# Kernel tuning notes

Measured on AMD Instinct MI355X. Metric: run time of the kernel, lower is better.

The kernel has to match this reference:

```python
import jax, jax.numpy as jnp
import numpy as np

B, C, N = 8, 128, 4096
C2 = C // 2
BN_EPS = 1e-5


def setup_inputs() -> dict:
    key = jax.random.key(0)
    ks = jax.random.split(key, 8)
    s = 1.0 / np.sqrt(C)
    s2 = 1.0 / np.sqrt(C2)
    return {
        "x": jax.random.normal(ks[0], (B, C, N), dtype=jnp.float32),
        "w_qk": jax.random.uniform(ks[1], (C2, C), jnp.float32, -s, s),  # shared q/k weight
        "w_v": jax.random.uniform(ks[2], (C2, C), jnp.float32, -s, s),
        "b_v": jax.random.uniform(ks[3], (C2,), jnp.float32, -s, s),
        "w_x": jax.random.uniform(ks[4], (C2, C), jnp.float32, -s, s),
        "w_t": jax.random.uniform(ks[5], (C2, C2), jnp.float32, -s2, s2),
        "b_t": jax.random.uniform(ks[6], (C2,), jnp.float32, -s2, s2),
        "gamma": jnp.ones((C2,), jnp.float32),
        "beta": jnp.zeros((C2,), jnp.float32),
    }


def reference(x, w_qk, w_v, b_v, w_x, w_t, b_t, gamma, beta):
    # 1x1 convs are per-point linear maps: [B,C,N] -> [B,C2,N]
    x_q = jnp.einsum("oc,bcn->bno", w_qk, x)          # [B, N, C2]
    x_k = jnp.einsum("oc,bcn->bon", w_qk, x)          # [B, C2, N]
    x_v = jnp.einsum("oc,bcn->bon", w_v, x) + b_v[None, :, None]

    energy = jnp.einsum("bno,bom->bnm", x_q, x_k)     # [B, N, N]
    attn = jax.nn.softmax(energy, axis=-1)            # row softmax
    attn = attn / (1e-9 + attn.sum(axis=1, keepdims=True))  # column L1 renorm

    x_r = jnp.einsum("bon,bnm->bom", x_v, attn)       # [B, C2, N]
    x_c = jnp.einsum("oc,bcn->bon", w_x, x)           # [B, C2, N]

    d = x_c - x_r
    t = jnp.einsum("oi,bin->bon", w_t, d) + b_t[None, :, None]
    # BatchNorm1d (training-mode batch stats) over (B, N) per channel
    mean = t.mean(axis=(0, 2), keepdims=True)
    var = t.var(axis=(0, 2), keepdims=True)
    t_hat = (t - mean) * jax.lax.rsqrt(var + BN_EPS)
    x_r2 = jax.nn.relu(gamma[None, :, None] * t_hat + beta[None, :, None])
    return x_c + x_r2
```

## Files before the change

### kernel.cpp

```cpp
#include <hip/hip_runtime.h>

#define B_   8
#define C_   128
#define N_   4096
#define C2_  64

typedef __bf16 bf16x8 __attribute__((ext_vector_type(8)));
typedef float  f32x4  __attribute__((ext_vector_type(4)));

#define MFMA16(a, b, c) __builtin_amdgcn_mfma_f32_16x16x32_bf16((a), (b), (c), 0, 0, 0)

#define QK_SCALE 1.2011224087864498f

static __device__ __forceinline__ unsigned short f2bf(float f) {
    union { __bf16 b; unsigned short u; } cv;
    cv.b = (__bf16)f;
    return cv.u;
}
static __device__ __forceinline__ float bf2f(unsigned short u) {
    union { unsigned int u; float f; } cv;
    cv.u = ((unsigned int)u) << 16;
    return cv.f;
}

struct us4 { unsigned short a, b, c, d; };

static __device__ __forceinline__ void gl_lds16(const unsigned short* g, void* l) {
    __builtin_amdgcn_global_load_lds(
        (const __attribute__((address_space(1))) unsigned int*)g,
        (__attribute__((address_space(3))) unsigned int*)l,
        16, 0, 0);
}

__global__ __launch_bounds__(256) void k1_proj(
    const float* __restrict__ x, const float* __restrict__ w_qk,
    const float* __restrict__ w_v, const float* __restrict__ b_v,
    const float* __restrict__ w_x,
    unsigned short* __restrict__ qk_t, unsigned short* __restrict__ xv_bf,
    float* __restrict__ xc)
{
    __shared__ __align__(16) unsigned short w_lds[192 * 136];
    __shared__ __align__(16) unsigned short x_t[64 * 136];
    const int tid = threadIdx.x;
    const int wave = tid >> 6, lane = tid & 63;
    const int quad = lane >> 4, col = lane & 15;
    const int b = blockIdx.y;
    const int n0 = blockIdx.x * 64;

    const float* wsrc[3] = {w_qk, w_v, w_x};
    #pragma unroll
    for (int mat = 0; mat < 3; ++mat) {
        const float* wm = wsrc[mat];
        #pragma unroll
        for (int it = 0; it < 8; ++it) {
            const int idx = it * 256 + tid;
            const int o = idx >> 5, c = (idx & 31) * 4;
            const float4 v = *(const float4*)(wm + o * C_ + c);
            us4 pk;
            pk.a = f2bf(v.x); pk.b = f2bf(v.y); pk.c = f2bf(v.z); pk.d = f2bf(v.w);
            *(us4*)&w_lds[(mat * 64 + o) * 136 + c] = pk;
        }
    }
    const float* xb = x + (size_t)b * C_ * N_ + n0;
    #pragma unroll
    for (int it = 0; it < 8; ++it) {
        const int idx = it * 256 + tid;
        const int c = idx >> 4, n = (idx & 15) * 4;
        const float4 v = *(const float4*)(xb + (size_t)c * N_ + n);
        x_t[(n + 0) * 136 + c] = f2bf(v.x);
        x_t[(n + 1) * 136 + c] = f2bf(v.y);
        x_t[(n + 2) * 136 + c] = f2bf(v.z);
        x_t[(n + 3) * 136 + c] = f2bf(v.w);
    }
    __syncthreads();

    const int nw = wave * 16;
    bf16x8 bfr[4];
    #pragma unroll
    for (int kt = 0; kt < 4; ++kt)
        bfr[kt] = *(const bf16x8*)&x_t[(nw + col) * 136 + kt * 32 + quad * 8];

    const int n_g = n0 + nw + col;

    #pragma unroll
    for (int ot = 0; ot < 12; ++ot) {
        f32x4 acc = {0.f, 0.f, 0.f, 0.f};
        #pragma unroll
        for (int kt = 0; kt < 4; ++kt) {
            const bf16x8 afr = *(const bf16x8*)&w_lds[(ot * 16 + col) * 136 + kt * 32 + quad * 8];
            acc = MFMA16(afr, bfr[kt], acc);
        }
        if (ot < 4) {
            us4 pk;
            pk.a = f2bf(acc[0] * QK_SCALE); pk.b = f2bf(acc[1] * QK_SCALE);
            pk.c = f2bf(acc[2] * QK_SCALE); pk.d = f2bf(acc[3] * QK_SCALE);
            *(us4*)&qk_t[(size_t)(b * N_ + n_g) * C2_ + ot * 16 + quad * 4] = pk;
        } else if (ot < 8) {
            const float4 bv4 = *(const float4*)(b_v + (ot - 4) * 16 + quad * 4);
            const float* bvp = (const float*)&bv4;
            #pragma unroll
            for (int r = 0; r < 4; ++r)
                xv_bf[(size_t)(b * C2_ + (ot - 4) * 16 + quad * 4 + r) * N_ + n_g]
                    = f2bf(acc[r] + bvp[r]);
        } else {
            #pragma unroll
            for (int r = 0; r < 4; ++r)
                xc[(size_t)(b * C2_ + (ot - 8) * 16 + quad * 4 + r) * N_ + n_g] = acc[r];
        }
    }
}

__global__ __launch_bounds__(256) void k2_rowstats(
    const unsigned short* __restrict__ qk_t, float* __restrict__ part_rs)
{
    __shared__ __align__(16) unsigned char lds_raw[2 * 8192];
    const int tid = threadIdx.x;
    const int wave = tid >> 6, lane = tid & 63;
    const int quad = lane >> 4, col = lane & 15;
    const int b = blockIdx.x & 7;
    const int nblk = (blockIdx.x >> 3) & 15;
    const int mq = blockIdx.x >> 7;
    const int n_base = nblk * 256 + wave * 64;
    const int m_start = mq * 512;
    const unsigned short* qb = qk_t + (size_t)b * N_ * C2_;

    bf16x8 a0[4], a1[4];
    #pragma unroll
    for (int s = 0; s < 4; ++s) {
        const unsigned short* p = qb + (size_t)(n_base + s * 16 + col) * C2_ + quad * 8;
        a0[s] = *(const bf16x8*)p;
        a1[s] = *(const bf16x8*)(p + 32);
    }

    auto stage = [&](int m0, int p) {
        unsigned char* base = lds_raw + p * 8192;
        #pragma unroll
        for (int r = 0; r < 2; ++r) {
            const int idx = r * 256 + tid;
            const int row = idx >> 3, seg = idx & 7;
            gl_lds16(qb + (size_t)(m0 + row) * C2_ + (size_t)(seg ^ (row & 7)) * 8,
                     base + idx * 16);
        }
    };

    float run_s[4][4];
    #pragma unroll
    for (int s = 0; s < 4; ++s)
        #pragma unroll
        for (int r = 0; r < 4; ++r) run_s[s][r] = 0.f;

    stage(m_start, 0);
    __syncthreads();

    for (int c = 0; c < 8; ++c) {
        const int p = c & 1;
        if (c + 1 < 8) stage(m_start + (c + 1) * 64, 1 - p);
        const unsigned short* qt = (const unsigned short*)(lds_raw + p * 8192);
        #pragma unroll
        for (int ms = 0; ms < 4; ++ms) {
            const int row = ms * 16 + col;
            const bf16x8 b0 = *(const bf16x8*)(qt + row * 64 + ((quad ^ (col & 7)) * 8));
            const bf16x8 b1 = *(const bf16x8*)(qt + row * 64 + (((4 + quad) ^ (col & 7)) * 8));
            #pragma unroll
            for (int s = 0; s < 4; ++s) {
                f32x4 acc = {0.f, 0.f, 0.f, 0.f};
                acc = MFMA16(a0[s], b0, acc);
                acc = MFMA16(a1[s], b1, acc);
                #pragma unroll
                for (int r = 0; r < 4; ++r)
                    run_s[s][r] += __builtin_amdgcn_exp2f(acc[r]);
            }
        }
        __syncthreads();
    }

    #pragma unroll
    for (int s = 0; s < 4; ++s)
        #pragma unroll
        for (int r = 0; r < 4; ++r) {
            #pragma unroll
            for (int off = 1; off < 16; off <<= 1)
                run_s[s][r] += __shfl_xor(run_s[s][r], off, 64);
        }
    if (col == 0) {
        #pragma unroll
        for (int s = 0; s < 4; ++s)
            #pragma unroll
            for (int r = 0; r < 4; ++r)
                part_rs[((size_t)(mq * 8 + b) << 12) + n_base + s * 16 + quad * 4 + r]
                    = run_s[s][r];
    }
}

__global__ __launch_bounds__(256) void k2b_comb(
    const float* __restrict__ part_rs, float* __restrict__ winv,
    unsigned short* __restrict__ wbf)
{
    const int i = blockIdx.x * 256 + threadIdx.x;
    const int b = i >> 12, n = i & 4095;
    float s = 0.f;
    #pragma unroll
    for (int q = 0; q < 8; ++q)
        s += part_rs[((size_t)(q * 8 + b) << 12) + n];
    const float w = 1.0f / s;
    winv[i] = w;
    wbf[i] = f2bf(w);
}

__global__ __launch_bounds__(256) void k2c_scale(
    unsigned short* __restrict__ xv_bf, const float* __restrict__ winv)
{
    const int t = blockIdx.x * 256 + threadIdx.x;
    const int flat = t * 4;
    const int b = flat >> 18;
    const int n = flat & 4095;
    const float4 w4 = *(const float4*)(winv + b * 4096 + n);
    us4 v = *(us4*)(xv_bf + flat);
    v.a = f2bf(bf2f(v.a) * w4.x);
    v.b = f2bf(bf2f(v.b) * w4.y);
    v.c = f2bf(bf2f(v.c) * w4.z);
    v.d = f2bf(bf2f(v.d) * w4.w);
    *(us4*)(xv_bf + flat) = v;
}

__global__ __launch_bounds__(256, 3) void k3_pv(
    const unsigned short* __restrict__ qk_t, const unsigned short* __restrict__ xv_bf,
    const unsigned short* __restrict__ wbf,
    float* __restrict__ yp0, float* __restrict__ yp1, float* __restrict__ yp2,
    float* __restrict__ cspart)
{
    __shared__ __align__(16) unsigned char lds_raw[32768 + 4 * 5120];
    const int tid = threadIdx.x;
    const int wave = tid >> 6, lane = tid & 63;
    const int quad = lane >> 4, col = lane & 15;
    const int nh2 = wave & 1, mh = wave >> 1;
    const int b = blockIdx.x & 7;
    const int m_blk = ((blockIdx.x >> 3) & 31) * 128;
    const int sk = blockIdx.x >> 8;
    const int n_start = (sk == 0) ? 0 : 1408 + (sk - 1) * 1344;
    const int n_chunks = (sk == 0) ? 22 : 21;
    const int m_wave = m_blk + mh * 64;
    const unsigned short* qb = qk_t + (size_t)b * N_ * C2_;
    const unsigned short* vb = xv_bf + (size_t)b * C2_ * N_;
    const unsigned short* wb = wbf + b * N_;
    float* yp = (sk == 0) ? yp0 : (sk == 1) ? yp1 : yp2;

    bf16x8 kb0[4], kb1[4];
    #pragma unroll
    for (int g = 0; g < 4; ++g) {
        const unsigned short* p = qb + (size_t)(m_wave + g * 16 + col) * C2_ + quad * 8;
        kb0[g] = *(const bf16x8*)p;
        kb1[g] = *(const bf16x8*)(p + 32);
    }

    unsigned short* stS = (unsigned short*)(lds_raw + 32768 + wave * 5120);

    auto stage = [&](int n0, int p) {
        unsigned char* qbase = lds_raw + p * 8192;
        unsigned char* vbase = lds_raw + 16384 + p * 8192;
        #pragma unroll
        for (int r = 0; r < 2; ++r) {
            const int idx = r * 256 + tid;
            const int row = idx >> 3, seg = idx & 7;
            const int ss = seg ^ (row & 7);
            gl_lds16(qb + (size_t)(n0 + row) * C2_ + (size_t)ss * 8, qbase + idx * 16);
            gl_lds16(vb + (size_t)row * N_ + n0 + ss * 8, vbase + idx * 16);
        }
    };

    f32x4 accY[4][4];
    #pragma unroll
    for (int g = 0; g < 4; ++g)
        #pragma unroll
        for (int os = 0; os < 4; ++os) accY[g][os] = (f32x4){0.f, 0.f, 0.f, 0.f};
    f32x4 csacc[4];
    #pragma unroll
    for (int g = 0; g < 4; ++g) csacc[g] = (f32x4){0.f, 0.f, 0.f, 0.f};

    stage(n_start, 0);
    __syncthreads();

    for (int c = 0; c < n_chunks; ++c) {
        const int n0 = n_start + c * 64;
        const int p = c & 1;
        if (c + 1 < n_chunks) stage(n0 + 64, 1 - p);

        const unsigned short* qt = (const unsigned short*)(lds_raw + p * 8192);
        const unsigned short* vt = (const unsigned short*)(lds_raw + 16384 + p * 8192);

        const bf16x8 wfrag = *(const bf16x8*)(wb + n0 + nh2 * 32 + quad * 8);

        #pragma unroll
        for (int ns = 0; ns < 2; ++ns) {
            const int row = nh2 * 32 + ns * 16 + col;
            const bf16x8 qa0 = *(const bf16x8*)(qt + row * 64 + ((quad ^ (col & 7)) * 8));
            const bf16x8 qa1 = *(const bf16x8*)(qt + row * 64 + (((4 + quad) ^ (col & 7)) * 8));
            #pragma unroll
            for (int g = 0; g < 4; ++g) {
                f32x4 acc = {0.f, 0.f, 0.f, 0.f};
                acc = MFMA16(qa0, kb0[g], acc);
                acc = MFMA16(qa1, kb1[g], acc);
                union { unsigned short us[4]; uint2 u2; } pk;
                #pragma unroll
                for (int r = 0; r < 4; ++r)
                    pk.us[r] = f2bf(__builtin_amdgcn_exp2f(acc[r]));
                *(uint2*)&stS[(g * 16 + col) * 40 + ns * 16 + quad * 4] = pk.u2;
            }
        }

        bf16x8 sB[4];
        #pragma unroll
        for (int g = 0; g < 4; ++g)
            sB[g] = *(const bf16x8*)&stS[(g * 16 + col) * 40 + quad * 8];

        #pragma unroll
        for (int g = 0; g < 4; ++g)
            csacc[g] = MFMA16(wfrag, sB[g], csacc[g]);

        #pragma unroll
        for (int os = 0; os < 4; ++os) {
            const bf16x8 va = *(const bf16x8*)(vt + (os * 16 + col) * 64 +
                                               (((nh2 * 4 + quad) ^ (col & 7)) * 8));
            #pragma unroll
            for (int g = 0; g < 4; ++g)
                accY[g][os] = MFMA16(va, sB[g], accY[g][os]);
        }
        __syncthreads();
    }

    float* cmb = (float*)lds_raw;
    float* csc = (float*)(lds_raw + 32768);
    if (nh2 == 1) {
        #pragma unroll
        for (int g = 0; g < 4; ++g) {
            #pragma unroll
            for (int os = 0; os < 4; ++os)
                #pragma unroll
                for (int r = 0; r < 4; ++r)
                    cmb[((mh * 16 + g * 4 + os) * 4 + r) * 64 + lane] = accY[g][os][r];
            csc[(mh * 4 + g) * 64 + lane] = csacc[g][0];
        }
    }
    __syncthreads();
    if (nh2 == 0) {
        #pragma unroll
        for (int g = 0; g < 4; ++g) {
            const float cs = csacc[g][0] + csc[(mh * 4 + g) * 64 + lane];
            if (lane < 16)
                cspart[((size_t)sk * 8 + b) * N_ + m_wave + g * 16 + lane] = cs;
            #pragma unroll
            for (int os = 0; os < 4; ++os)
                #pragma unroll
                for (int r = 0; r < 4; ++r) {
                    const float v = accY[g][os][r] +
                        cmb[((mh * 16 + g * 4 + os) * 4 + r) * 64 + lane];
                    yp[(size_t)(b * C2_ + os * 16 + quad * 4 + r) * N_ + m_wave + g * 16 + col] = v;
                }
        }
    }
}

__global__ __launch_bounds__(256) void k3b_comb(
    float* yp0, const float* __restrict__ yp1, const float* __restrict__ yp2,
    const float* __restrict__ cspart)
{
    const int idx4 = blockIdx.x * 256 + threadIdx.x;
    const int b = idx4 >> 16;
    const int m4 = idx4 & 1023;
    const float4 y0 = ((const float4*)yp0)[idx4];
    const float4 y1 = ((const float4*)yp1)[idx4];
    const float4 y2 = ((const float4*)yp2)[idx4];
    const float4 c0 = ((const float4*)cspart)[b * 1024 + m4];
    const float4 c1 = ((const float4*)cspart)[8192 + b * 1024 + m4];
    const float4 c2 = ((const float4*)cspart)[16384 + b * 1024 + m4];
    float4 r;
    r.x = (y0.x + y1.x + y2.x) / (1e-9f + c0.x + c1.x + c2.x);
    r.y = (y0.y + y1.y + y2.y) / (1e-9f + c0.y + c1.y + c2.y);
    r.z = (y0.z + y1.z + y2.z) / (1e-9f + c0.z + c1.z + c2.z);
    r.w = (y0.w + y1.w + y2.w) / (1e-9f + c0.w + c1.w + c2.w);
    ((float4*)yp0)[idx4] = r;
}

__global__ __launch_bounds__(256) void k4_t(
    const float* __restrict__ xc, const float* __restrict__ xr,
    const float* __restrict__ w_t, const float* __restrict__ b_t,
    float* __restrict__ t_buf)
{
    __shared__ float d_lds[64][64];
    __shared__ float w_lds[64][64];
    const int b = blockIdx.y;
    const int n0 = blockIdx.x * 64;
    const size_t base = (size_t)b * C2_ * N_;

    for (int idx = threadIdx.x; idx < 4096; idx += 256) {
        const int i = idx >> 6, n = idx & 63;
        const size_t g = base + (size_t)i * N_ + n0 + n;
        d_lds[i][n] = xc[g] - xr[g];
        w_lds[i][n] = w_t[idx];
    }
    __syncthreads();

    const int n = threadIdx.x & 63, ow = (threadIdx.x >> 6) * 16;
    float acc[16];
    #pragma unroll
    for (int oo = 0; oo < 16; ++oo) acc[oo] = 0.f;
    for (int i = 0; i < 64; ++i) {
        const float dv = d_lds[i][n];
        #pragma unroll
        for (int oo = 0; oo < 16; ++oo)
            acc[oo] += w_lds[ow + oo][i] * dv;
    }
    #pragma unroll
    for (int oo = 0; oo < 16; ++oo)
        t_buf[base + (size_t)(ow + oo) * N_ + n0 + n] = acc[oo] + b_t[ow + oo];
}

__global__ __launch_bounds__(256) void k5_bnstats(
    const float* __restrict__ t_buf, float* __restrict__ bn)
{
    const int o = blockIdx.x;
    float s = 0.f, s2 = 0.f;
    for (int b = 0; b < B_; ++b) {
        const float4* p = (const float4*)(t_buf + (size_t)(b * C2_ + o) * N_);
        for (int j = threadIdx.x; j < N_ / 4; j += 256) {
            const float4 v = p[j];
            s  += v.x + v.y + v.z + v.w;
            s2 += v.x * v.x + v.y * v.y + v.z * v.z + v.w * v.w;
        }
    }
    #pragma unroll
    for (int off = 1; off < 64; off <<= 1) {
        s  += __shfl_xor(s, off, 64);
        s2 += __shfl_xor(s2, off, 64);
    }
    __shared__ float red[2][4];
    if ((threadIdx.x & 63) == 0) {
        red[0][threadIdx.x >> 6] = s;
        red[1][threadIdx.x >> 6] = s2;
    }
    __syncthreads();
    if (threadIdx.x == 0) {
        bn[o]       = red[0][0] + red[0][1] + red[0][2] + red[0][3];
        bn[64 + o]  = red[1][0] + red[1][1] + red[1][2] + red[1][3];
    }
}

__global__ __launch_bounds__(256) void k6_out(
    const float* __restrict__ xc, const float* __restrict__ t_buf,
    const float* __restrict__ bn, const float* __restrict__ gamma,
    const float* __restrict__ beta, float* __restrict__ out)
{
    const int idx = blockIdx.x * 256 + threadIdx.x;
    const int o = (idx >> 10) & 63;
    const float invC = 1.0f / (float)(B_ * N_);
    const float mean = bn[o] * invC;
    const float var  = bn[64 + o] * invC - mean * mean;
    const float sc = gamma[o] * rsqrtf(var + 1e-5f);
    const float sh = beta[o] - mean * sc;
    const float4 t4 = ((const float4*)t_buf)[idx];
    const float4 c4 = ((const float4*)xc)[idx];
    float4 r;
    r.x = c4.x + fmaxf(0.f, sc * t4.x + sh);
    r.y = c4.y + fmaxf(0.f, sc * t4.y + sh);
    r.z = c4.z + fmaxf(0.f, sc * t4.z + sh);
    r.w = c4.w + fmaxf(0.f, sc * t4.w + sh);
    ((float4*)out)[idx] = r;
}

extern "C" void kernel_launch(void* const* d_in, const int* in_sizes, int n_in,
                              void* d_out, int out_size, void* d_ws, size_t ws_size,
                              hipStream_t stream) {
    const float* x     = (const float*)d_in[0];
    const float* w_qk  = (const float*)d_in[1];
    const float* w_v   = (const float*)d_in[2];
    const float* b_v   = (const float*)d_in[3];
    const float* w_x   = (const float*)d_in[4];
    const float* w_t   = (const float*)d_in[5];
    const float* b_t   = (const float*)d_in[6];
    const float* gamma = (const float*)d_in[7];
    const float* beta  = (const float*)d_in[8];
    float* out = (float*)d_out;

    char* ws = (char*)d_ws;
    unsigned short* qk_t  = (unsigned short*)ws;
    unsigned short* xv_bf = (unsigned short*)(ws + (4  << 20));
    float* xc      = (float*)(ws + (8  << 20));
    float* xr_yp0  = (float*)(ws + (16 << 20));
    float* tb_yp1  = (float*)(ws + (24 << 20));
    float* part_rs = (float*)(ws + (32 << 20));
    float* cspart  = (float*)(ws + (32 << 20));
    float* winv    = (float*)(ws + (33 << 20));
    unsigned short* wbf = (unsigned short*)(ws + (33 << 20) + (128 << 10));
    float* bn      = (float*)(ws + (33 << 20) + (192 << 10));
    float* yp2     = out;

    hipLaunchKernelGGL(k1_proj,     dim3(64, 8),  256, 0, stream,
                       x, w_qk, w_v, b_v, w_x, qk_t, xv_bf, xc);
    hipLaunchKernelGGL(k2_rowstats, dim3(1024),   256, 0, stream, qk_t, part_rs);
    hipLaunchKernelGGL(k2b_comb,    dim3(128),    256, 0, stream, part_rs, winv, wbf);
    hipLaunchKernelGGL(k2c_scale,   dim3(2048),   256, 0, stream, xv_bf, winv);
    hipLaunchKernelGGL(k3_pv,       dim3(768),    256, 0, stream,
                       qk_t, xv_bf, wbf, xr_yp0, tb_yp1, yp2, cspart);
    hipLaunchKernelGGL(k3b_comb,    dim3(2048),   256, 0, stream, xr_yp0, tb_yp1, yp2, cspart);
    hipLaunchKernelGGL(k4_t,        dim3(64, 8),  256, 0, stream, xc, xr_yp0, w_t, b_t, tb_yp1);
    hipLaunchKernelGGL(k5_bnstats,  dim3(64),     256, 0, stream, tb_yp1, bn);
    hipLaunchKernelGGL(k6_out,      dim3(2048),   256, 0, stream, xc, tb_yp1, bn, gamma, beta, out);
}
```

Measured before the change: 192.7 us.

## Fuse combine, scaling and BN-stat kernels; use MFMA for the transform conv

Merges the row-sum combine and the V-scaling kernels into one kernel that keeps per-column weights in LDS. Folds the split-K combine and column renormalisation into the transform kernel, which now runs its 64x64 matmul on bf16 MFMA and emits partial BatchNorm sums, so the full-tensor stats pass becomes a small reduction over partials. The row-stats kernel now stages 128-row chunks instead of 64. The intent is fewer launches and fewer full passes over the intermediates, at the cost of bf16 rounding of the difference tensor and in-place aliasing of y1 with t_buf.

```diff
diff --git a/kernel.cpp b/kernel.cpp
--- a/kernel.cpp
+++ b/kernel.cpp
@@ -113,7 +113,7 @@
 __global__ __launch_bounds__(256) void k2_rowstats(
     const unsigned short* __restrict__ qk_t, float* __restrict__ part_rs)
 {
-    __shared__ __align__(16) unsigned char lds_raw[2 * 8192];
+    __shared__ __align__(16) unsigned char lds_raw[2 * 16384];
     const int tid = threadIdx.x;
     const int wave = tid >> 6, lane = tid & 63;
     const int quad = lane >> 4, col = lane & 15;
@@ -133,9 +133,9 @@
     }
 
     auto stage = [&](int m0, int p) {
-        unsigned char* base = lds_raw + p * 8192;
-        #pragma unroll
-        for (int r = 0; r < 2; ++r) {
+        unsigned char* base = lds_raw + p * 16384;
+        #pragma unroll
+        for (int r = 0; r < 4; ++r) {
             const int idx = r * 256 + tid;
             const int row = idx >> 3, seg = idx & 7;
             gl_lds16(qb + (size_t)(m0 + row) * C2_ + (size_t)(seg ^ (row & 7)) * 8,
@@ -152,12 +152,12 @@
     stage(m_start, 0);
     __syncthreads();
 
-    for (int c = 0; c < 8; ++c) {
+    for (int c = 0; c < 4; ++c) {
         const int p = c & 1;
-        if (c + 1 < 8) stage(m_start + (c + 1) * 64, 1 - p);
-        const unsigned short* qt = (const unsigned short*)(lds_raw + p * 8192);
-        #pragma unroll
-        for (int ms = 0; ms < 4; ++ms) {
+        if (c + 1 < 4) stage(m_start + (c + 1) * 128, 1 - p);
+        const unsigned short* qt = (const unsigned short*)(lds_raw + p * 16384);
+        #pragma unroll
+        for (int ms = 0; ms < 8; ++ms) {
             const int row = ms * 16 + col;
             const bf16x8 b0 = *(const bf16x8*)(qt + row * 64 + ((quad ^ (col & 7)) * 8));
             const bf16x8 b1 = *(const bf16x8*)(qt + row * 64 + (((4 + quad) ^ (col & 7)) * 8));
@@ -192,35 +192,36 @@
     }
 }
 
-__global__ __launch_bounds__(256) void k2b_comb(
-    const float* __restrict__ part_rs, float* __restrict__ winv,
+__global__ __launch_bounds__(256) void k2bc(
+    const float* __restrict__ part_rs, unsigned short* __restrict__ xv_bf,
     unsigned short* __restrict__ wbf)
 {
-    const int i = blockIdx.x * 256 + threadIdx.x;
-    const int b = i >> 12, n = i & 4095;
-    float s = 0.f;
-    #pragma unroll
-    for (int q = 0; q < 8; ++q)
-        s += part_rs[((size_t)(q * 8 + b) << 12) + n];
-    const float w = 1.0f / s;
-    winv[i] = w;
-    wbf[i] = f2bf(w);
-}
-
-__global__ __launch_bounds__(256) void k2c_scale(
-    unsigned short* __restrict__ xv_bf, const float* __restrict__ winv)
-{
-    const int t = blockIdx.x * 256 + threadIdx.x;
-    const int flat = t * 4;
-    const int b = flat >> 18;
-    const int n = flat & 4095;
-    const float4 w4 = *(const float4*)(winv + b * 4096 + n);
-    us4 v = *(us4*)(xv_bf + flat);
-    v.a = f2bf(bf2f(v.a) * w4.x);
-    v.b = f2bf(bf2f(v.b) * w4.y);
-    v.c = f2bf(bf2f(v.c) * w4.z);
-    v.d = f2bf(bf2f(v.d) * w4.w);
-    *(us4*)(xv_bf + flat) = v;
+    __shared__ float wl[64];
+    const int tid = threadIdx.x;
+    const int b = blockIdx.x & 7;
+    const int n0 = (blockIdx.x >> 3) * 64;
+    if (tid < 64) {
+        float s = 0.f;
+        #pragma unroll
+        for (int q = 0; q < 8; ++q)
+            s += part_rs[((size_t)(q * 8 + b) << 12) + n0 + tid];
+        const float w = 1.0f / s;
+        wl[tid] = w;
+        wbf[b * N_ + n0 + tid] = f2bf(w);
+    }
+    __syncthreads();
+    #pragma unroll
+    for (int it = 0; it < 4; ++it) {
+        const int idx4 = it * 256 + tid;
+        const int o = idx4 >> 4, n4 = (idx4 & 15) * 4;
+        unsigned short* p = xv_bf + (size_t)(b * C2_ + o) * N_ + n0 + n4;
+        us4 v = *(us4*)p;
+        v.a = f2bf(bf2f(v.a) * wl[n4 + 0]);
+        v.b = f2bf(bf2f(v.b) * wl[n4 + 1]);
+        v.c = f2bf(bf2f(v.c) * wl[n4 + 2]);
+        v.d = f2bf(bf2f(v.d) * wl[n4 + 3]);
+        *(us4*)p = v;
+    }
 }
 
 __global__ __launch_bounds__(256, 3) void k3_pv(
@@ -360,89 +361,112 @@
     }
 }
 
-__global__ __launch_bounds__(256) void k3b_comb(
-    float* yp0, const float* __restrict__ yp1, const float* __restrict__ yp2,
-    const float* __restrict__ cspart)
-{
-    const int idx4 = blockIdx.x * 256 + threadIdx.x;
-    const int b = idx4 >> 16;
-    const int m4 = idx4 & 1023;
-    const float4 y0 = ((const float4*)yp0)[idx4];
-    const float4 y1 = ((const float4*)yp1)[idx4];
-    const float4 y2 = ((const float4*)yp2)[idx4];
-    const float4 c0 = ((const float4*)cspart)[b * 1024 + m4];
-    const float4 c1 = ((const float4*)cspart)[8192 + b * 1024 + m4];
-    const float4 c2 = ((const float4*)cspart)[16384 + b * 1024 + m4];
-    float4 r;
-    r.x = (y0.x + y1.x + y2.x) / (1e-9f + c0.x + c1.x + c2.x);
-    r.y = (y0.y + y1.y + y2.y) / (1e-9f + c0.y + c1.y + c2.y);
-    r.z = (y0.z + y1.z + y2.z) / (1e-9f + c0.z + c1.z + c2.z);
-    r.w = (y0.w + y1.w + y2.w) / (1e-9f + c0.w + c1.w + c2.w);
-    ((float4*)yp0)[idx4] = r;
-}
-
 __global__ __launch_bounds__(256) void k4_t(
-    const float* __restrict__ xc, const float* __restrict__ xr,
-    const float* __restrict__ w_t, const float* __restrict__ b_t,
-    float* __restrict__ t_buf)
-{
-    __shared__ float d_lds[64][64];
-    __shared__ float w_lds[64][64];
+    const float* __restrict__ xc, const float* __restrict__ y0,
+    const float* __restrict__ y1, const float* __restrict__ y2,
+    const float* __restrict__ cspart, const float* __restrict__ w_t,
+    const float* __restrict__ b_t, float* __restrict__ t_buf,
+    float* __restrict__ part_bn)
+{
+    __shared__ __align__(16) unsigned short wlds[64 * 72];
+    __shared__ __align__(16) unsigned short d_t[64 * 72];
+    __shared__ float cinv[64];
+    const int tid = threadIdx.x;
+    const int wave = tid >> 6, lane = tid & 63;
+    const int quad = lane >> 4, col = lane & 15;
     const int b = blockIdx.y;
     const int n0 = blockIdx.x * 64;
     const size_t base = (size_t)b * C2_ * N_;
 
-    for (int idx = threadIdx.x; idx < 4096; idx += 256) {
-        const int i = idx >> 6, n = idx & 63;
-        const size_t g = base + (size_t)i * N_ + n0 + n;
-        d_lds[i][n] = xc[g] - xr[g];
-        w_lds[i][n] = w_t[idx];
-    }
-    __syncthreads();
-
-    const int n = threadIdx.x & 63, ow = (threadIdx.x >> 6) * 16;
-    float acc[16];
-    #pragma unroll
-    for (int oo = 0; oo < 16; ++oo) acc[oo] = 0.f;
-    for (int i = 0; i < 64; ++i) {
-        const float dv = d_lds[i][n];
-        #pragma unroll
-        for (int oo = 0; oo < 16; ++oo)
-            acc[oo] += w_lds[ow + oo][i] * dv;
-    }
-    #pragma unroll
-    for (int oo = 0; oo < 16; ++oo)
-        t_buf[base + (size_t)(ow + oo) * N_ + n0 + n] = acc[oo] + b_t[ow + oo];
-}
-
-__global__ __launch_bounds__(256) void k5_bnstats(
-    const float* __restrict__ t_buf, float* __restrict__ bn)
-{
-    const int o = blockIdx.x;
-    float s = 0.f, s2 = 0.f;
-    for (int b = 0; b < B_; ++b) {
-        const float4* p = (const float4*)(t_buf + (size_t)(b * C2_ + o) * N_);
-        for (int j = threadIdx.x; j < N_ / 4; j += 256) {
-            const float4 v = p[j];
-            s  += v.x + v.y + v.z + v.w;
-            s2 += v.x * v.x + v.y * v.y + v.z * v.z + v.w * v.w;
-        }
-    }
-    #pragma unroll
-    for (int off = 1; off < 64; off <<= 1) {
-        s  += __shfl_xor(s, off, 64);
-        s2 += __shfl_xor(s2, off, 64);
-    }
-    __shared__ float red[2][4];
-    if ((threadIdx.x & 63) == 0) {
-        red[0][threadIdx.x >> 6] = s;
-        red[1][threadIdx.x >> 6] = s2;
-    }
-    __syncthreads();
-    if (threadIdx.x == 0) {
-        bn[o]       = red[0][0] + red[0][1] + red[0][2] + red[0][3];
-        bn[64 + o]  = red[1][0] + red[1][1] + red[1][2] + red[1][3];
-    }
+    #pragma unroll
+    for (int it = 0; it < 4; ++it) {
+        const int idx4 = it * 256 + tid;
+        const int o = idx4 >> 4, i4 = (idx4 & 15) * 4;
+        const float4 v = *(const float4*)(w_t + o * 64 + i4);
+        us4 pk;
+        pk.a = f2bf(v.x); pk.b = f2bf(v.y); pk.c = f2bf(v.z); pk.d = f2bf(v.w);
+        *(us4*)&wlds[o * 72 + i4] = pk;
+    }
+    if (tid < 64) {
+        const int n = n0 + tid;
+        const float cs = cspart[(size_t)b * N_ + n] + cspart[(size_t)(8 + b) * N_ + n]
+                       + cspart[(size_t)(16 + b) * N_ + n];
+        cinv[tid] = 1.0f / (1e-9f + cs);
+    }
+    __syncthreads();
+
+    #pragma unroll
+    for (int it = 0; it < 4; ++it) {
+        const int idx4 = it * 256 + tid;
+        const int i = idx4 >> 4, n4 = (idx4 & 15) * 4;
+        const size_t g = base + (size_t)i * N_ + n0 + n4;
+        const float4 c4 = *(const float4*)(xc + g);
+        const float4 a0 = *(const float4*)(y0 + g);
+        const float4 a1 = *(const float4*)(y1 + g);
+        const float4 a2 = *(const float4*)(y2 + g);
+        d_t[(n4 + 0) * 72 + i] = f2bf(c4.x - (a0.x + a1.x + a2.x) * cinv[n4 + 0]);
+        d_t[(n4 + 1) * 72 + i] = f2bf(c4.y - (a0.y + a1.y + a2.y) * cinv[n4 + 1]);
+        d_t[(n4 + 2) * 72 + i] = f2bf(c4.z - (a0.z + a1.z + a2.z) * cinv[n4 + 2]);
+        d_t[(n4 + 3) * 72 + i] = f2bf(c4.w - (a0.w + a1.w + a2.w) * cinv[n4 + 3]);
+    }
+    __syncthreads();
+
+    const int ow = wave * 16;
+    bf16x8 afr[2];
+    #pragma unroll
+    for (int kt = 0; kt < 2; ++kt)
+        afr[kt] = *(const bf16x8*)&wlds[(ow + col) * 72 + kt * 32 + quad * 8];
+    const float4 bt4 = *(const float4*)(b_t + ow + quad * 4);
+    const float* btp = (const float*)&bt4;
+
+    float s[4] = {0.f, 0.f, 0.f, 0.f}, q2[4] = {0.f, 0.f, 0.f, 0.f};
+    #pragma unroll
+    for (int ns = 0; ns < 4; ++ns) {
+        f32x4 acc = {0.f, 0.f, 0.f, 0.f};
+        #pragma unroll
+        for (int kt = 0; kt < 2; ++kt) {
+            const bf16x8 bfr = *(const bf16x8*)&d_t[(ns * 16 + col) * 72 + kt * 32 + quad * 8];
+            acc = MFMA16(afr[kt], bfr, acc);
+        }
+        #pragma unroll
+        for (int r = 0; r < 4; ++r) {
+            const float t = acc[r] + btp[r];
+            t_buf[base + (size_t)(ow + quad * 4 + r) * N_ + n0 + ns * 16 + col] = t;
+            s[r] += t;
+            q2[r] += t * t;
+        }
+    }
+    #pragma unroll
+    for (int r = 0; r < 4; ++r) {
+        #pragma unroll
+        for (int off = 1; off < 16; off <<= 1) {
+            s[r]  += __shfl_xor(s[r],  off, 64);
+            q2[r] += __shfl_xor(q2[r], off, 64);
+        }
+    }
+    if (col == 0) {
+        const int blk = blockIdx.x * 8 + b;
+        #pragma unroll
+        for (int r = 0; r < 4; ++r) {
+            part_bn[(size_t)(ow + quad * 4 + r) * 512 + blk]      = s[r];
+            part_bn[(size_t)(64 + ow + quad * 4 + r) * 512 + blk] = q2[r];
+        }
+    }
+}
+
+__global__ __launch_bounds__(256) void k5r(
+    const float* __restrict__ part_bn, float* __restrict__ bn)
+{
+    const int c = blockIdx.x;
+    const int tid = threadIdx.x, wave = tid >> 6, lane = tid & 63;
+    float s = 0.f;
+    for (int j = tid; j < 512; j += 256) s += part_bn[(size_t)c * 512 + j];
+    #pragma unroll
+    for (int off = 1; off < 64; off <<= 1) s += __shfl_xor(s, off, 64);
+    __shared__ float red[4];
+    if (lane == 0) red[wave] = s;
+    __syncthreads();
+    if (tid == 0) bn[c] = red[0] + red[1] + red[2] + red[3];
 }
 
 __global__ __launch_bounds__(256) void k6_out(
@@ -485,24 +509,23 @@
     unsigned short* qk_t  = (unsigned short*)ws;
     unsigned short* xv_bf = (unsigned short*)(ws + (4  << 20));
     float* xc      = (float*)(ws + (8  << 20));
-    float* xr_yp0  = (float*)(ws + (16 << 20));
+    float* yp0     = (float*)(ws + (16 << 20));
     float* tb_yp1  = (float*)(ws + (24 << 20));
     float* part_rs = (float*)(ws + (32 << 20));
     float* cspart  = (float*)(ws + (32 << 20));
-    float* winv    = (float*)(ws + (33 << 20));
-    unsigned short* wbf = (unsigned short*)(ws + (33 << 20) + (128 << 10));
-    float* bn      = (float*)(ws + (33 << 20) + (192 << 10));
+    unsigned short* wbf = (unsigned short*)(ws + (33 << 20));
+    float* part_bn = (float*)(ws + (33 << 20) + (64 << 10));
+    float* bn      = (float*)(ws + (33 << 20) + (320 << 10));
     float* yp2     = out;
 
     hipLaunchKernelGGL(k1_proj,     dim3(64, 8),  256, 0, stream,
                        x, w_qk, w_v, b_v, w_x, qk_t, xv_bf, xc);
     hipLaunchKernelGGL(k2_rowstats, dim3(1024),   256, 0, stream, qk_t, part_rs);
-    hipLaunchKernelGGL(k2b_comb,    dim3(128),    256, 0, stream, part_rs, winv, wbf);
-    hipLaunchKernelGGL(k2c_scale,   dim3(2048),   256, 0, stream, xv_bf, winv);
+    hipLaunchKernelGGL(k2bc,        dim3(512),    256, 0, stream, part_rs, xv_bf, wbf);
     hipLaunchKernelGGL(k3_pv,       dim3(768),    256, 0, stream,
-                       qk_t, xv_bf, wbf, xr_yp0, tb_yp1, yp2, cspart);
-    hipLaunchKernelGGL(k3b_comb,    dim3(2048),   256, 0, stream, xr_yp0, tb_yp1, yp2, cspart);
-    hipLaunchKernelGGL(k4_t,        dim3(64, 8),  256, 0, stream, xc, xr_yp0, w_t, b_t, tb_yp1);
-    hipLaunchKernelGGL(k5_bnstats,  dim3(64),     256, 0, stream, tb_yp1, bn);
+                       qk_t, xv_bf, wbf, yp0, tb_yp1, yp2, cspart);
+    hipLaunchKernelGGL(k4_t,        dim3(64, 8),  256, 0, stream,
+                       xc, yp0, tb_yp1, yp2, cspart, w_t, b_t, tb_yp1, part_bn);
+    hipLaunchKernelGGL(k5r,         dim3(128),    256, 0, stream, part_bn, bn);
     hipLaunchKernelGGL(k6_out,      dim3(2048),   256, 0, stream, xc, tb_yp1, bn, gamma, beta, out);
 }
```

New measurement: 168.9 us. 12.3% less time.
